# Kernel tuning notes

Measured on AMD Instinct MI355X. Metric: run time of the kernel, lower is better.

## Reference

```python
import jax, jax.numpy as jnp
import numpy as np

B, T, U = 4, 256, 64
D_ENC = D_PRED = 512
JOINT = 1024
VOCAB = 1024


def setup_inputs() -> dict:
    key = jax.random.key(0)
    ks = jax.random.split(key, 8)
    s = lambda d: 1.0 / np.sqrt(d)
    return {
        "enc": jax.random.normal(ks[0], (B, T, D_ENC), jnp.float32),
        "pred": jax.random.normal(ks[1], (B, U, D_PRED), jnp.float32),
        "W_enc": jax.random.normal(ks[2], (D_ENC, JOINT), jnp.float32) * s(D_ENC),
        "b_enc": jnp.zeros((JOINT,), jnp.float32),
        "W_pred": jax.random.normal(ks[3], (D_PRED, JOINT), jnp.float32) * s(D_PRED),
        "b_pred": jnp.zeros((JOINT,), jnp.float32),
        "W_out": jax.random.normal(ks[4], (JOINT, VOCAB), jnp.float32) * s(JOINT),
        "b_out": jnp.zeros((VOCAB,), jnp.float32),
    }


def reference(enc, pred, W_enc, b_enc, W_pred, b_pred, W_out, b_out):
    # Dense projections to joint_dim
    enc_out = jnp.einsum("btd,dj->btj", enc, W_enc) + b_enc      # [B,T,J]
    pred_out = jnp.einsum("bud,dj->buj", pred, W_pred) + b_pred  # [B,U,J]
    # Broadcast add over (T,U), tanh, then vocab projection
    joint = jnp.tanh(enc_out[:, :, None, :] + pred_out[:, None, :, :])  # [B,T,U,J]
    logits = jnp.einsum("btuj,jv->btuv", joint, W_out) + b_out           # [B,T,U,V]
    return logits
```

## Files before the change

### kernel.cpp

```cpp
#include <hip/hip_runtime.h>
#include <hip/hip_bf16.h>


typedef __bf16 bf16x8 __attribute__((ext_vector_type(8)));
typedef float f32x4 __attribute__((ext_vector_type(4)));
typedef unsigned int u32x4 __attribute__((ext_vector_type(4)));
using bf16_t = __hip_bfloat16;

#define B_ 4
#define T_ 256
#define U_ 64
#define DE 512
#define JD 1024
#define VV 1024

__device__ __forceinline__ void gl2lds16(const void* g, void* l) {
  __builtin_amdgcn_global_load_lds(
      (__attribute__((address_space(1))) void*)(g),
      (__attribute__((address_space(3))) void*)(l), 16, 0, 0);
}

__device__ __forceinline__ float fast_tanh(float x) {
  float xx = fminf(fmaxf(x, -30.f), 30.f);
  float e = __expf(2.f * xx);
  return 1.f - 2.f * __builtin_amdgcn_rcpf(e + 1.f);
}

__device__ __forceinline__ void transpose_body(const float* __restrict__ src,
                                               bf16_t* __restrict__ dst,
                                               int K, int N, int bx, int by, int tid,
                                               float (*tile)[33]) {
  const int nt = bx * 32, kt = by * 32;
  const int tx = tid & 31, ty = tid >> 5;
#pragma unroll
  for (int i = 0; i < 4; ++i)
    tile[ty + i * 8][tx] = src[(size_t)(kt + ty + i * 8) * N + nt + tx];
  __syncthreads();
#pragma unroll
  for (int i = 0; i < 4; ++i)
    dst[(size_t)(nt + ty + i * 8) * K + kt + tx] = __float2bfloat16(tile[tx][ty + i * 8]);
}

__global__ __launch_bounds__(256) void prep_k(
    const float* __restrict__ enc, const float* __restrict__ pred,
    bf16_t* __restrict__ encb, bf16_t* __restrict__ predb,
    const float* __restrict__ W_enc, bf16_t* __restrict__ WtE,
    const float* __restrict__ W_pred, bf16_t* __restrict__ WtP,
    const float* __restrict__ W_out, bf16_t* __restrict__ WtO) {
  __shared__ float tile[32][33];
  const int bid = blockIdx.x, tid = threadIdx.x;
  if (bid < 640) {
    size_t i = ((size_t)bid * 256 + tid) * 4;
    const float* src;
    bf16_t* dst;
    if (i < (size_t)B_ * T_ * DE) { src = enc; dst = encb; }
    else { i -= (size_t)B_ * T_ * DE; src = pred; dst = predb; }
    f32x4 v = *(const f32x4*)(src + i);
    bf16_t o[4];
#pragma unroll
    for (int z = 0; z < 4; ++z) o[z] = __float2bfloat16(v[z]);
    *(unsigned long long*)(dst + i) = *(unsigned long long*)o;
  } else if (bid < 1152) {
    const int lb = bid - 640;
    transpose_body(W_enc, WtE, DE, JD, lb & 31, lb >> 5, tid, tile);
  } else if (bid < 1664) {
    const int lb = bid - 1152;
    transpose_body(W_pred, WtP, DE, JD, lb & 31, lb >> 5, tid, tile);
  } else {
    const int lb = bid - 1664;
    transpose_body(W_out, WtO, JD, VV, lb & 31, lb >> 5, tid, tile);
  }
}

__device__ __forceinline__ void proj_body(const bf16_t* __restrict__ A,
                                          const bf16_t* __restrict__ Bt,
                                          const float* __restrict__ bias,
                                          float* __restrict__ C,
                                          int m0, int n0, int N, int K) {
  __shared__ bf16_t sA[128 * 32];
  __shared__ bf16_t sB[128 * 32];
  const int tid = threadIdx.x;
  const int wave = tid >> 6, lane = tid & 63;
  const int wm = wave >> 1, wn = wave & 1;

  f32x4 acc[4][4] = {};

  for (int k0 = 0; k0 < K; k0 += 32) {
    __syncthreads();
#pragma unroll
    for (int r = 0; r < 2; ++r) {
      const int base = (wave + 4 * r) * 1024;
      const int row  = (base >> 6) + (lane >> 2);
      const int kel  = (lane & 3) * 8;
      gl2lds16(A  + (size_t)(m0 + row) * K + k0 + kel, (char*)sA + base);
      gl2lds16(Bt + (size_t)(n0 + row) * K + k0 + kel, (char*)sB + base);
    }
    __syncthreads();
    bf16x8 af[4], bfr[4];
    const int kq = (lane >> 4) * 8;
#pragma unroll
    for (int i = 0; i < 4; ++i) {
      af[i]  = *(const bf16x8*)(const void*)(sA + (wm * 64 + i * 16 + (lane & 15)) * 32 + kq);
      bfr[i] = *(const bf16x8*)(const void*)(sB + (wn * 64 + i * 16 + (lane & 15)) * 32 + kq);
    }
#pragma unroll
    for (int i = 0; i < 4; ++i)
#pragma unroll
      for (int j = 0; j < 4; ++j)
        acc[i][j] = __builtin_amdgcn_mfma_f32_16x16x32_bf16(af[i], bfr[j], acc[i][j], 0, 0, 0);
  }

  float bv[4];
#pragma unroll
  for (int j = 0; j < 4; ++j) bv[j] = bias[n0 + wn * 64 + j * 16 + (lane & 15)];
#pragma unroll
  for (int i = 0; i < 4; ++i) {
    const int row = m0 + wm * 64 + i * 16 + ((lane >> 4) << 2);
#pragma unroll
    for (int j = 0; j < 4; ++j) {
      const int col = n0 + wn * 64 + j * 16 + (lane & 15);
#pragma unroll
      for (int rr = 0; rr < 4; ++rr)
        C[(size_t)(row + rr) * N + col] = acc[i][j][rr] + bv[j];
    }
  }
}

__global__ __launch_bounds__(256) void proj2_k(
    const bf16_t* __restrict__ encb, const bf16_t* __restrict__ predb,
    const bf16_t* __restrict__ WtE, const bf16_t* __restrict__ WtP,
    const float* __restrict__ b_enc, const float* __restrict__ b_pred,
    float* __restrict__ enc_o, float* __restrict__ pred_o) {
  int bid = blockIdx.x;
  if (bid < 64) {
    proj_body(encb, WtE, b_enc, enc_o, (bid >> 3) * 128, (bid & 7) * 128, JD, DE);
  } else {
    bid -= 64;
    proj_body(predb, WtP, b_pred, pred_o, (bid >> 3) * 128, (bid & 7) * 128, JD, DE);
  }
}

__global__ __launch_bounds__(256) void tanh_mat_k(
    const float* __restrict__ enc_o,
    const float* __restrict__ pred_o,
    bf16_t* __restrict__ joint) {
  size_t i = ((size_t)blockIdx.x * 256 + threadIdx.x) * 8;
  const int m = (int)(i >> 10);
  const int j = (int)(i & 1023);
  const int enc_row  = m >> 6;
  const int pred_row = ((m >> 14) << 6) | (m & 63);
  const f32x4* pe = (const f32x4*)(enc_o  + (size_t)enc_row  * JD + j);
  const f32x4* pp = (const f32x4*)(pred_o + (size_t)pred_row * JD + j);
  bf16_t vals[8];
#pragma unroll
  for (int q = 0; q < 2; ++q) {
    f32x4 e = pe[q], p = pp[q];
#pragma unroll
    for (int z = 0; z < 4; ++z)
      vals[q * 4 + z] = __float2bfloat16(fast_tanh(e[z] + p[z]));
  }
  *(u32x4*)(void*)(joint + i) = *(const u32x4*)(const void*)vals;
}


struct RS { u32x4 v[4]; };

__global__ __launch_bounds__(512, 2) void vocab_gemm9_k(
    const bf16_t* __restrict__ A,
    const bf16_t* __restrict__ Bt,
    const float* __restrict__ bias,
    float* __restrict__ C) {
  __shared__ char smem[65536];
  const int tid  = threadIdx.x;
  const int wave = tid >> 6, lane = tid & 63;
  const int wm = wave >> 2, wn = wave & 3;

  const int cpx = gridDim.x >> 3;
  const int b   = blockIdx.x;
  const int lb  = (b & 7) * cpx + (b >> 3);
  const int n0  = (lb & 3) * 256;
  const int m0  = (lb >> 2) * 256;

  const int ra  = tid >> 1;
  const int c0  = (tid & 1) * 2;
  const int key = (ra >> 1) & 3;
  const bf16_t* pa = A  + (size_t)(m0 + ra) * JD;
  const bf16_t* pb = Bt + (size_t)(n0 + ra) * JD;
  const int go0 = c0 * 8, go1 = (c0 + 1) * 8;
  const int lo0 = ((c0 ^ key)) * 16, lo1 = ((c0 + 1) ^ key) * 16;

  char* abuf[2] = { smem, smem + 32768 };

  f32x4 acc[8][4] = {};
  const int NT = JD / 32;

#define ISSUE(S, K0)                                           \
  do {                                                         \
    (S).v[0] = *(const u32x4*)(const void*)(pa + (K0) + go0);  \
    (S).v[1] = *(const u32x4*)(const void*)(pa + (K0) + go1);  \
    (S).v[2] = *(const u32x4*)(const void*)(pb + (K0) + go0);  \
    (S).v[3] = *(const u32x4*)(const void*)(pb + (K0) + go1);  \
  } while (0)

#define WRITE(S, AB)                                           \
  do {                                                         \
    char* ab_ = (AB);                                          \
    *(u32x4*)(void*)(ab_ + ra * 64 + lo0)         = (S).v[0];  \
    *(u32x4*)(void*)(ab_ + ra * 64 + lo1)         = (S).v[1];  \
    *(u32x4*)(void*)(ab_ + 16384 + ra * 64 + lo0) = (S).v[2];  \
    *(u32x4*)(void*)(ab_ + 16384 + ra * 64 + lo1) = (S).v[3];  \
  } while (0)

#define BOUND()                                                \
  do {                                                         \
    asm volatile("s_waitcnt lgkmcnt(0)" ::: "memory");         \
    __builtin_amdgcn_s_barrier();                              \
    __builtin_amdgcn_sched_barrier(0);                         \
  } while (0)

#define CONSUME(AB)                                                            \
  do {                                                                         \
    const char* ab_ = (AB);                                                    \
    const char* bb_ = ab_ + 16384;                                             \
    const int kq = lane >> 4;                                                  \
    bf16x8 bfr[4];                                                             \
    _Pragma("unroll")                                                          \
    for (int j = 0; j < 4; ++j) {                                              \
      const int rb = wn * 64 + j * 16 + (lane & 15);                           \
      const int cb = kq ^ ((rb >> 1) & 3);                                     \
      bfr[j] = *(const bf16x8*)(const void*)(bb_ + rb * 64 + cb * 16);         \
    }                                                                          \
    _Pragma("unroll")                                                          \
    for (int mh = 0; mh < 2; ++mh) {                                           \
      bf16x8 af[4];                                                            \
      _Pragma("unroll")                                                        \
      for (int i = 0; i < 4; ++i) {                                            \
        const int rr_ = wm * 128 + mh * 64 + i * 16 + (lane & 15);             \
        const int ca = kq ^ ((rr_ >> 1) & 3);                                  \
        af[i] = *(const bf16x8*)(const void*)(ab_ + rr_ * 64 + ca * 16);       \
      }                                                                        \
      __builtin_amdgcn_s_setprio(1);                                           \
      _Pragma("unroll")                                                        \
      for (int i = 0; i < 4; ++i)                                              \
        _Pragma("unroll")                                                      \
        for (int j = 0; j < 4; ++j)                                            \
          acc[mh * 4 + i][j] = __builtin_amdgcn_mfma_f32_16x16x32_bf16(        \
              af[i], bfr[j], acc[mh * 4 + i][j], 0, 0, 0);                     \
      __builtin_amdgcn_s_setprio(0);                                           \
    }                                                                          \
  } while (0)

  RS rsE, rsO;
  ISSUE(rsE, 0);
  ISSUE(rsO, 32);
  WRITE(rsE, abuf[0]);
  BOUND();

  for (int t = 0; t < NT; t += 2) {
    if (t + 2 < NT) ISSUE(rsE, (t + 2) * 32);
    CONSUME(abuf[0]);
    WRITE(rsO, abuf[1]);
    BOUND();
    if (t + 3 < NT) ISSUE(rsO, (t + 3) * 32);
    CONSUME(abuf[1]);
    if (t + 2 < NT) {
      WRITE(rsE, abuf[0]);
      BOUND();
    }
  }

#undef ISSUE
#undef WRITE
#undef BOUND
#undef CONSUME

  float bv[4];
#pragma unroll
  for (int j = 0; j < 4; ++j) bv[j] = bias[n0 + wn * 64 + j * 16 + (lane & 15)];
#pragma unroll
  for (int i = 0; i < 8; ++i) {
    const int row = m0 + wm * 128 + i * 16 + ((lane >> 4) << 2);
#pragma unroll
    for (int j = 0; j < 4; ++j) {
      const int col = n0 + wn * 64 + j * 16 + (lane & 15);
#pragma unroll
      for (int rr = 0; rr < 4; ++rr)
        C[(size_t)(row + rr) * VV + col] = acc[i][j][rr] + bv[j];
    }
  }
}

extern "C" void kernel_launch(void* const* d_in, const int* in_sizes, int n_in,
                              void* d_out, int out_size, void* d_ws, size_t ws_size,
                              hipStream_t stream) {
  const float* enc    = (const float*)d_in[0];
  const float* pred   = (const float*)d_in[1];
  const float* W_enc  = (const float*)d_in[2];
  const float* b_enc  = (const float*)d_in[3];
  const float* W_pred = (const float*)d_in[4];
  const float* b_pred = (const float*)d_in[5];
  const float* W_out  = (const float*)d_in[6];
  const float* b_out  = (const float*)d_in[7];
  float* out = (float*)d_out;

  char* ws = (char*)d_ws;
  bf16_t* encb   = (bf16_t*)(ws + 0x000000);
  bf16_t* predb  = (bf16_t*)(ws + 0x100000);
  bf16_t* WtE    = (bf16_t*)(ws + 0x140000);
  bf16_t* WtP    = (bf16_t*)(ws + 0x240000);
  bf16_t* WtO    = (bf16_t*)(ws + 0x340000);
  float*  enc_o  = (float*) (ws + 0x540000);
  float*  pred_o = (float*) (ws + 0x940000);
  bf16_t* joint  = (bf16_t*)(ws + 0xA40000);

  prep_k<<<2688, 256, 0, stream>>>(enc, pred, encb, predb, W_enc, WtE, W_pred, WtP, W_out, WtO);
  proj2_k<<<80, 256, 0, stream>>>(encb, predb, WtE, WtP, b_enc, b_pred, enc_o, pred_o);
  tanh_mat_k<<<(B_*T_*U_) * JD / (8 * 256), 256, 0, stream>>>(enc_o, pred_o, joint);
  vocab_gemm9_k<<<dim3(((B_*T_*U_) / 256) * (VV / 256)), 512, 0, stream>>>(
      joint, WtO, b_out, out);
}
```

Baseline: 462.8 us.

## Rewrite vocab GEMM main loop with direct global-to-LDS loads and quadrant-interleaved pipeline

The vocab GEMM no longer stages tiles through registers and then LDS. It uses global_load_lds to write A and B tiles straight into a double-buffered, swizzled LDS layout. Each K-step is split into four MFMA quadrants, with LDS fragment reads, partial next-tile prefetches and barriers interleaved between them, in an 8-wave ping-pong schedule. This is meant to cut VGPR pressure and LDS write instructions and to overlap memory traffic with MFMA work, at the cost of many more barriers per step and delicate vmcnt accounting.

```diff
diff --git a/kernel.cpp b/kernel.cpp
--- a/kernel.cpp
+++ b/kernel.cpp
@@ -163,9 +163,7 @@
 }
 
 
-struct RS { u32x4 v[4]; };
-
-__global__ __launch_bounds__(512, 2) void vocab_gemm9_k(
+__global__ __launch_bounds__(512, 2) void vocab_gemm10_k(
     const bf16_t* __restrict__ A,
     const bf16_t* __restrict__ Bt,
     const float* __restrict__ bias,
@@ -181,98 +179,115 @@
   const int n0  = (lb & 3) * 256;
   const int m0  = (lb >> 2) * 256;
 
-  const int ra  = tid >> 1;
-  const int c0  = (tid & 1) * 2;
-  const int key = (ra >> 1) & 3;
-  const bf16_t* pa = A  + (size_t)(m0 + ra) * JD;
-  const bf16_t* pb = Bt + (size_t)(n0 + ra) * JD;
-  const int go0 = c0 * 8, go1 = (c0 + 1) * 8;
-  const int lo0 = ((c0 ^ key)) * 16, lo1 = ((c0 + 1) ^ key) * 16;
-
-  char* abuf[2] = { smem, smem + 32768 };
+  const int sr  = wave * 16 + (lane >> 2);
+  const int scg = (lane & 3) ^ ((sr >> 1) & 3);
+  const int ldst = wave * 1024 + lane * 16;
+  const bf16_t* gA0 = A  + (size_t)(m0 + sr)       * JD + scg * 8;
+  const bf16_t* gA1 = A  + (size_t)(m0 + 128 + sr) * JD + scg * 8;
+  const bf16_t* gB0 = Bt + (size_t)(n0 + sr)       * JD + scg * 8;
+  const bf16_t* gB1 = Bt + (size_t)(n0 + 128 + sr) * JD + scg * 8;
+
+  const int sl = lane & 15, ql = lane >> 4;
 
   f32x4 acc[8][4] = {};
+  bf16x8 af[4], bf[2];
   const int NT = JD / 32;
 
-#define ISSUE(S, K0)                                           \
-  do {                                                         \
-    (S).v[0] = *(const u32x4*)(const void*)(pa + (K0) + go0);  \
-    (S).v[1] = *(const u32x4*)(const void*)(pa + (K0) + go1);  \
-    (S).v[2] = *(const u32x4*)(const void*)(pb + (K0) + go0);  \
-    (S).v[3] = *(const u32x4*)(const void*)(pb + (K0) + go1);  \
-  } while (0)
-
-#define WRITE(S, AB)                                           \
-  do {                                                         \
-    char* ab_ = (AB);                                          \
-    *(u32x4*)(void*)(ab_ + ra * 64 + lo0)         = (S).v[0];  \
-    *(u32x4*)(void*)(ab_ + ra * 64 + lo1)         = (S).v[1];  \
-    *(u32x4*)(void*)(ab_ + 16384 + ra * 64 + lo0) = (S).v[2];  \
-    *(u32x4*)(void*)(ab_ + 16384 + ra * 64 + lo1) = (S).v[3];  \
-  } while (0)
-
-#define BOUND()                                                \
-  do {                                                         \
-    asm volatile("s_waitcnt lgkmcnt(0)" ::: "memory");         \
-    __builtin_amdgcn_s_barrier();                              \
-    __builtin_amdgcn_sched_barrier(0);                         \
-  } while (0)
-
-#define CONSUME(AB)                                                            \
-  do {                                                                         \
-    const char* ab_ = (AB);                                                    \
-    const char* bb_ = ab_ + 16384;                                             \
-    const int kq = lane >> 4;                                                  \
-    bf16x8 bfr[4];                                                             \
-    _Pragma("unroll")                                                          \
-    for (int j = 0; j < 4; ++j) {                                              \
-      const int rb = wn * 64 + j * 16 + (lane & 15);                           \
-      const int cb = kq ^ ((rb >> 1) & 3);                                     \
-      bfr[j] = *(const bf16x8*)(const void*)(bb_ + rb * 64 + cb * 16);         \
-    }                                                                          \
-    _Pragma("unroll")                                                          \
-    for (int mh = 0; mh < 2; ++mh) {                                           \
-      bf16x8 af[4];                                                            \
-      _Pragma("unroll")                                                        \
-      for (int i = 0; i < 4; ++i) {                                            \
-        const int rr_ = wm * 128 + mh * 64 + i * 16 + (lane & 15);             \
-        const int ca = kq ^ ((rr_ >> 1) & 3);                                  \
-        af[i] = *(const bf16x8*)(const void*)(ab_ + rr_ * 64 + ca * 16);       \
-      }                                                                        \
-      __builtin_amdgcn_s_setprio(1);                                           \
-      _Pragma("unroll")                                                        \
-      for (int i = 0; i < 4; ++i)                                              \
-        _Pragma("unroll")                                                      \
-        for (int j = 0; j < 4; ++j)                                            \
-          acc[mh * 4 + i][j] = __builtin_amdgcn_mfma_f32_16x16x32_bf16(        \
-              af[i], bfr[j], acc[mh * 4 + i][j], 0, 0, 0);                     \
-      __builtin_amdgcn_s_setprio(0);                                           \
-    }                                                                          \
-  } while (0)
-
-  RS rsE, rsO;
-  ISSUE(rsE, 0);
-  ISSUE(rsO, 32);
-  WRITE(rsE, abuf[0]);
-  BOUND();
-
-  for (int t = 0; t < NT; t += 2) {
-    if (t + 2 < NT) ISSUE(rsE, (t + 2) * 32);
-    CONSUME(abuf[0]);
-    WRITE(rsO, abuf[1]);
-    BOUND();
-    if (t + 3 < NT) ISSUE(rsO, (t + 3) * 32);
-    CONSUME(abuf[1]);
-    if (t + 2 < NT) {
-      WRITE(rsE, abuf[0]);
-      BOUND();
-    }
-  }
-
-#undef ISSUE
-#undef WRITE
-#undef BOUND
-#undef CONSUME
+#define STAGE(D, H, S)                                                        \
+  do {                                                                        \
+    const bf16_t* g_ = ((H) == 0 ? gA0 : (H) == 1 ? gA1 : (H) == 2 ? gB0 : gB1) + (S) * 32; \
+    gl2lds16(g_, smem + (D) * 32768 + (H) * 8192 + ldst);                     \
+  } while (0)
+
+#define LOAD_AF(D, QM)                                                        \
+  do {                                                                        \
+    _Pragma("unroll")                                                         \
+    for (int i = 0; i < 4; ++i) {                                             \
+      const int lr = (QM) * 64 + i * 16 + sl;                                 \
+      af[i] = *(const bf16x8*)(const void*)(                                  \
+          smem + (D) * 32768 + wm * 8192 + lr * 64 + ((ql ^ ((lr >> 1) & 3)) * 16)); \
+    }                                                                         \
+  } while (0)
+
+#define LOAD_BF(D, QN)                                                        \
+  do {                                                                        \
+    _Pragma("unroll")                                                         \
+    for (int jj = 0; jj < 2; ++jj) {                                          \
+      const int lr = (wn & 1) * 64 + ((QN) * 2 + jj) * 16 + sl;               \
+      bf[jj] = *(const bf16x8*)(const void*)(                                 \
+          smem + (D) * 32768 + 16384 + (wn >> 1) * 8192 + lr * 64 +           \
+          ((ql ^ ((lr >> 1) & 3)) * 16));                                     \
+    }                                                                         \
+  } while (0)
+
+#define MFMA_Q(QM, QN)                                                        \
+  do {                                                                        \
+    __builtin_amdgcn_s_setprio(1);                                            \
+    _Pragma("unroll")                                                         \
+    for (int i = 0; i < 4; ++i)                                               \
+      _Pragma("unroll")                                                       \
+      for (int jj = 0; jj < 2; ++jj)                                          \
+        acc[(QM) * 4 + i][(QN) * 2 + jj] = __builtin_amdgcn_mfma_f32_16x16x32_bf16( \
+            af[i], bf[jj], acc[(QM) * 4 + i][(QN) * 2 + jj], 0, 0, 0);        \
+    __builtin_amdgcn_s_setprio(0);                                            \
+  } while (0)
+
+#define BAR1()                                                                \
+  do {                                                                        \
+    __builtin_amdgcn_s_barrier();                                             \
+    asm volatile("s_waitcnt lgkmcnt(0)" ::: "memory");                        \
+    __builtin_amdgcn_sched_barrier(0);                                        \
+  } while (0)
+
+#define BAR2()                                                                \
+  do {                                                                        \
+    __builtin_amdgcn_s_barrier();                                             \
+    __builtin_amdgcn_sched_barrier(0);                                        \
+  } while (0)
+
+#define STEP(D, S)                                                            \
+  do {                                                                        \
+    const int s_ = (S);                                                       \
+                                                              \
+    LOAD_AF(D, 0); LOAD_BF(D, 0);                                             \
+    if (s_ + 1 < NT) STAGE((D) ^ 1, 2, s_ + 1);                               \
+    BAR1(); MFMA_Q(0, 0); BAR2();                                             \
+                                                              \
+    LOAD_BF(D, 1);                                                            \
+    if (s_ + 1 < NT) STAGE((D) ^ 1, 3, s_ + 1);                               \
+    BAR1(); MFMA_Q(0, 1); BAR2();                                             \
+                                                              \
+    LOAD_AF(D, 1);                                                            \
+    BAR1(); MFMA_Q(1, 1); BAR2();                                             \
+                                                              \
+    LOAD_BF(D, 0);                                                            \
+    if (s_ + 2 < NT) { STAGE(D, 0, s_ + 2); STAGE(D, 1, s_ + 2); }            \
+    BAR1(); MFMA_Q(1, 0);                                                     \
+    if (s_ + 1 < NT) {                                                        \
+      if (s_ + 2 < NT) asm volatile("s_waitcnt vmcnt(2)" ::: "memory");       \
+      else             asm volatile("s_waitcnt vmcnt(0)" ::: "memory");       \
+      BAR2();                                                                 \
+    }                                                                         \
+  } while (0)
+
+  STAGE(0, 0, 0); STAGE(0, 1, 0); STAGE(0, 2, 0); STAGE(0, 3, 0);
+  STAGE(1, 0, 1); STAGE(1, 1, 1);
+  asm volatile("s_waitcnt vmcnt(2)" ::: "memory");
+  __builtin_amdgcn_s_barrier();
+  __builtin_amdgcn_sched_barrier(0);
+
+  for (int it = 0; it < NT / 2; ++it) {
+    STEP(0, 2 * it);
+    STEP(1, 2 * it + 1);
+  }
+
+#undef STAGE
+#undef LOAD_AF
+#undef LOAD_BF
+#undef MFMA_Q
+#undef BAR1
+#undef BAR2
+#undef STEP
 
   float bv[4];
 #pragma unroll
@@ -316,6 +331,6 @@
   prep_k<<<2688, 256, 0, stream>>>(enc, pred, encb, predb, W_enc, WtE, W_pred, WtP, W_out, WtO);
   proj2_k<<<80, 256, 0, stream>>>(encb, predb, WtE, WtP, b_enc, b_pred, enc_o, pred_o);
   tanh_mat_k<<<(B_*T_*U_) * JD / (8 * 256), 256, 0, stream>>>(enc_o, pred_o, joint);
-  vocab_gemm9_k<<<dim3(((B_*T_*U_) / 256) * (VV / 256)), 512, 0, stream>>>(
+  vocab_gemm10_k<<<dim3(((B_*T_*U_) / 256) * (VV / 256)), 512, 0, stream>>>(
       joint, WtO, b_out, out);
 }
```

New measurement: 435.9 us. 1.06x faster.
